# Kernel optimization log

Hardware: AMD Instinct MI355X
Metric: run time of the kernel (lower is better)

The kernel has to match this reference:

```python
import jax, jax.numpy as jnp
import numpy as np

NUM_NODES = 100000
NUM_EDGES = 1200000
DIM = 64
NUM_LAYERS = 3
NUM_GRAPHS = 512
BN_EPS = 1e-5


def setup_inputs() -> dict:
    key = jax.random.key(0)
    ks = jax.random.split(key, 12)
    x = jax.random.normal(ks[0], (NUM_NODES, DIM), dtype=jnp.float32)
    edge_index = jax.random.randint(ks[1], (2, NUM_EDGES), 0, NUM_NODES, dtype=jnp.int64)
    edge_weight = jax.random.uniform(ks[2], (NUM_EDGES,), dtype=jnp.float32)
    batch = jnp.sort(jax.random.randint(ks[3], (NUM_NODES,), 0, NUM_GRAPHS, dtype=jnp.int64))
    W1 = jax.random.normal(ks[4], (NUM_LAYERS, DIM, DIM), dtype=jnp.float32) * 0.1
    b1 = jax.random.normal(ks[5], (NUM_LAYERS, DIM), dtype=jnp.float32) * 0.1
    W2 = jax.random.normal(ks[6], (NUM_LAYERS, DIM, DIM), dtype=jnp.float32) * 0.1
    b2 = jax.random.normal(ks[7], (NUM_LAYERS, DIM), dtype=jnp.float32) * 0.1
    gamma = jax.random.uniform(ks[8], (NUM_LAYERS, DIM), dtype=jnp.float32) + 0.5
    beta = jax.random.normal(ks[9], (NUM_LAYERS, DIM), dtype=jnp.float32) * 0.1
    return {"x": x, "edge_index": edge_index, "edge_weight": edge_weight,
            "batch": batch, "pool": 0, "W1": W1, "b1": b1, "W2": W2,
            "b2": b2, "gamma": gamma, "beta": beta}


def reference(x, edge_index, edge_weight, batch, pool, W1, b1, W2, b2, gamma, beta):
    # WGINConv (eps=0): h = MLP(x + scatter_add(edge_weight * x[src] -> dst))
    # then ReLU, then BatchNorm1d in training mode (batch statistics).
    src, dst = edge_index[0], edge_index[1]
    n_nodes = x.shape[0]
    xs = []
    for i in range(W1.shape[0]):
        msg = x[src] * edge_weight[:, None]                       # [E, D] gather
        agg = jax.ops.segment_sum(msg, dst, num_segments=n_nodes)  # [N, D] scatter-add
        h = agg + x                                                # (1+eps)*x, eps=0
        h = jax.nn.relu(h @ W1[i].T + b1[i]) @ W2[i].T + b2[i]     # GIN MLP
        h = jax.nn.relu(h)
        mu = h.mean(0)
        var = ((h - mu) ** 2).mean(0)                              # biased var (BN train)
        x = gamma[i] * (h - mu) * jax.lax.rsqrt(var + BN_EPS) + beta[i]
        xs.append(x)
    if pool == 0:  # 'add' pooling (static python int)
        xpool = [jax.ops.segment_sum(v, batch, num_segments=NUM_GRAPHS) for v in xs]
    else:          # 'mean' pooling
        counts = jax.ops.segment_sum(jnp.ones((n_nodes,), x.dtype), batch,
                                     num_segments=NUM_GRAPHS)
        denom = jnp.maximum(counts, 1.0)[:, None]
        xpool = [jax.ops.segment_sum(v, batch, num_segments=NUM_GRAPHS) / denom for v in xs]
    return (jnp.concatenate(xpool, axis=1), jnp.concatenate(xs, axis=1))
```

## Files before the change

kernel.cpp:

```cpp
#include <hip/hip_runtime.h>

#define N_NODES 100000
#define N_EDGES 1200000
#define DIM     64
#define N_LAYERS 3
#define N_GRAPHS 512
#define OUTD    192
#define BN_EPS  1e-5f

#define NPB 64
#define LDS_PITCH 65
#define NLBLK ((N_NODES + NPB - 1) / NPB)

#define BSHIFT 9
#define BUCK_NODES (1 << BSHIFT)
#define NBUK ((N_NODES + BUCK_NODES - 1) / BUCK_NODES)
#define EPB 4096
#define NPBLK ((N_EDGES + EPB - 1) / EPB)

__global__ void transpose_w(const float* __restrict__ W1, const float* __restrict__ W2,
                            float* __restrict__ W1T, float* __restrict__ W2T,
                            float* __restrict__ idaff) {
    int idx = blockIdx.x * blockDim.x + threadIdx.x;
    if (idx < 128) idaff[idx] = (idx < 64) ? 1.0f : 0.0f;
    if (idx >= N_LAYERS * DIM * DIM) return;
    int l = idx >> 12;
    int r = idx & 4095;
    int j = r >> 6;
    int k = r & 63;
    int dstp = (l << 12) + k * DIM + j;
    W1T[dstp] = W1[idx];
    W2T[dstp] = W2[idx];
}

__global__ void __launch_bounds__(256) part_hist(const int* __restrict__ dst,
                                                 int* __restrict__ hist,
                                                 int* __restrict__ tot) {
    __shared__ int h[NBUK];
    int t = threadIdx.x;
    if (t < NBUK) h[t] = 0;
    __syncthreads();
    int base = blockIdx.x * EPB;
    for (int i = t; i < EPB; i += 256) {
        int e = base + i;
        if (e < N_EDGES) atomicAdd(&h[dst[e] >> BSHIFT], 1);
    }
    __syncthreads();
    if (t < NBUK) {
        int v = h[t];
        hist[blockIdx.x * NBUK + t] = v;
        if (v) atomicAdd(&tot[t], v);
    }
}

__global__ void __launch_bounds__(256) scan196(const int* __restrict__ tot,
                                               int* __restrict__ bstart) {
    __shared__ int lds[256];
    int t = threadIdx.x;
    int v = (t < NBUK) ? tot[t] : 0;
    lds[t] = v;
    __syncthreads();
    for (int o = 1; o < 256; o <<= 1) {
        int add = (t >= o) ? lds[t - o] : 0;
        __syncthreads();
        lds[t] += add;
        __syncthreads();
    }
    if (t < NBUK) bstart[t] = lds[t] - v;
    if (t == 0) bstart[NBUK] = N_EDGES;
}

__global__ void __launch_bounds__(256) base_fill(const int* __restrict__ hist,
                                                 const int* __restrict__ bstart,
                                                 int* __restrict__ base) {
    __shared__ int c[512];
    __shared__ int ssum[256];
    int b = blockIdx.x, t = threadIdx.x;
    c[t] = (t < NPBLK) ? hist[t * NBUK + b] : 0;
    c[t + 256] = (t + 256 < NPBLK) ? hist[(t + 256) * NBUK + b] : 0;
    __syncthreads();
    int c0 = c[2 * t], c1 = c[2 * t + 1];
    int ps = c0 + c1;
    ssum[t] = ps;
    __syncthreads();
    int v = ps;
    for (int o = 1; o < 256; o <<= 1) {
        int add = (t >= o) ? ssum[t - o] : 0;
        __syncthreads();
        ssum[t] += add;
        __syncthreads();
    }
    int excl = ssum[t] - v + bstart[b];
    if (2 * t < NPBLK)     base[(2 * t) * NBUK + b] = excl;
    if (2 * t + 1 < NPBLK) base[(2 * t + 1) * NBUK + b] = excl + c0;
}

__global__ void __launch_bounds__(256) part_scatter(
        const int* __restrict__ src, const int* __restrict__ dst,
        const float* __restrict__ ew, const int* __restrict__ base,
        int2* __restrict__ pp) {
    __shared__ int cur[NBUK];
    int t = threadIdx.x;
    if (t < NBUK) cur[t] = base[blockIdx.x * NBUK + t];
    __syncthreads();
    int bb = blockIdx.x * EPB;
    for (int i = t; i < EPB; i += 256) {
        int e = bb + i;
        if (e < N_EDGES) {
            int d = dst[e];
            int bk = d >> BSHIFT;
            int pos = atomicAdd(&cur[bk], 1);
            int dl = d & (BUCK_NODES - 1);
            pp[pos] = make_int2(src[e] | (dl << 17), __float_as_int(ew[e]));
        }
    }
}

__global__ void __launch_bounds__(256) csr_build(
        const int2* __restrict__ pp, const int* __restrict__ bstart,
        int* __restrict__ seg, int2* __restrict__ pe) {
    __shared__ int cnt[BUCK_NODES];
    __shared__ int ssum[256];
    int b = blockIdx.x, t = threadIdx.x;
    int ebeg = bstart[b], eend = bstart[b + 1];
    cnt[t] = 0;
    cnt[t + 256] = 0;
    __syncthreads();
    for (int e = ebeg + t; e < eend; e += 256)
        atomicAdd(&cnt[pp[e].x >> 17], 1);
    __syncthreads();
    int c0 = cnt[2 * t], c1 = cnt[2 * t + 1];
    int ps = c0 + c1;
    ssum[t] = ps;
    __syncthreads();
    int v = ps;
    for (int o = 1; o < 256; o <<= 1) {
        int add = (t >= o) ? ssum[t - o] : 0;
        __syncthreads();
        ssum[t] += add;
        __syncthreads();
    }
    int excl = ssum[t] - v;
    int o0 = ebeg + excl;
    int o1 = o0 + c0;
    int n0 = (b << BSHIFT) + 2 * t;
    if (n0 < N_NODES) seg[n0] = o0;
    if (n0 + 1 < N_NODES) seg[n0 + 1] = o1;
    __syncthreads();
    cnt[2 * t] = o0;
    cnt[2 * t + 1] = o1;
    __syncthreads();
    for (int e = ebeg + t; e < eend; e += 256) {
        int2 p = pp[e];
        int pos = atomicAdd(&cnt[p.x >> 17], 1);
        pe[pos] = make_int2(p.x & 0x1FFFF, p.y);
    }
    if (b == 0 && t == 0) seg[N_NODES] = N_EDGES;
}

__global__ void __launch_bounds__(256) layer_kernel(
    const float* __restrict__ x_in, int xstride,
    const int* __restrict__ seg,
    const int2* __restrict__ pe,
    const float* __restrict__ affine ,
    const float* __restrict__ W1T, const float* __restrict__ b1,
    const float* __restrict__ W2T, const float* __restrict__ b2,
    float* __restrict__ out ,
    float* __restrict__ pstat ) {
    __shared__ float lds[NPB * LDS_PITCH];
    int t = threadIdx.x;
    int lane = t & 63;
    int wid = __builtin_amdgcn_readfirstlane(t >> 6);
    int nbase = blockIdx.x * NPB;

    int slot = lane >> 4;
    int col  = lane & 15;
    const float4* aff4 = (const float4*)affine;
    float4 sc4 = aff4[col];
    float4 sh4 = aff4[16 + col];

    for (int nn = 0; nn < 16; ++nn) {
        int nl = wid * 16 + nn;
        int n = nbase + nl;
        float ax = 0.f, ay = 0.f, az = 0.f, aw = 0.f, wsa = 0.f;
        float bx = 0.f, by = 0.f, bz = 0.f, bw = 0.f, wsb = 0.f;
        if (n < N_NODES) {
            int beg = seg[n];
            int end = seg[n + 1];
#define GBODY(EI, X, Y, Z, W, WS)                                              \
            if ((EI) < end) {                                                  \
                int2 p = pe[EI];                                               \
                float w = __int_as_float(p.y);                                 \
                const float4* rp =                                             \
                    (const float4*)(x_in + (size_t)p.x * xstride) + col;       \
                float4 v = *rp;                                                \
                X = fmaf(w, v.x, X); Y = fmaf(w, v.y, Y);                      \
                Z = fmaf(w, v.z, Z); W = fmaf(w, v.w, W);                      \
                WS += w;                                                       \
            }
            for (int e = beg; e < end; e += 16) {
                int e0 = e + slot;
                GBODY(e0,      ax, ay, az, aw, wsa)
                GBODY(e0 + 4,  bx, by, bz, bw, wsb)
                GBODY(e0 + 8,  ax, ay, az, aw, wsa)
                GBODY(e0 + 12, bx, by, bz, bw, wsb)
            }
#undef GBODY
        }
        float sx = ax + bx, sy = ay + by, sz = az + bz, sw = aw + bw;
        float ws = wsa + wsb;
        sx += __shfl_xor(sx, 16); sy += __shfl_xor(sy, 16);
        sz += __shfl_xor(sz, 16); sw += __shfl_xor(sw, 16);
        ws += __shfl_xor(ws, 16);
        sx += __shfl_xor(sx, 32); sy += __shfl_xor(sy, 32);
        sz += __shfl_xor(sz, 32); sw += __shfl_xor(sw, 32);
        ws += __shfl_xor(ws, 32);
        if (lane < 16) {
            float r0 = 0.f, r1 = 0.f, r2 = 0.f, r3 = 0.f;
            if (n < N_NODES) {
                const float4* xr =
                    (const float4*)(x_in + (size_t)n * xstride) + col;
                float4 s = *xr;
                float shw = 1.0f + ws;
                r0 = fmaf(sc4.x, sx + s.x, sh4.x * shw);
                r1 = fmaf(sc4.y, sy + s.y, sh4.y * shw);
                r2 = fmaf(sc4.z, sz + s.z, sh4.z * shw);
                r3 = fmaf(sc4.w, sw + s.w, sh4.w * shw);
            }
            int lb = nl * LDS_PITCH + col * 4;
            lds[lb] = r0; lds[lb + 1] = r1; lds[lb + 2] = r2; lds[lb + 3] = r3;
        }
    }
    __syncthreads();

    float h[16];
#pragma unroll
    for (int jj = 0; jj < 16; ++jj) h[jj] = b1[wid * 16 + jj];
#pragma unroll 4
    for (int k = 0; k < DIM; ++k) {
        float xv = lds[lane * LDS_PITCH + k];
        const float* wr = W1T + k * DIM + wid * 16;
#pragma unroll
        for (int jj = 0; jj < 16; ++jj) h[jj] = fmaf(xv, wr[jj], h[jj]);
    }
#pragma unroll
    for (int jj = 0; jj < 16; ++jj) h[jj] = fmaxf(h[jj], 0.0f);
    __syncthreads();
#pragma unroll
    for (int jj = 0; jj < 16; ++jj) lds[lane * LDS_PITCH + wid * 16 + jj] = h[jj];
    __syncthreads();

    float o[16];
#pragma unroll
    for (int jj = 0; jj < 16; ++jj) o[jj] = b2[wid * 16 + jj];
#pragma unroll 4
    for (int k = 0; k < DIM; ++k) {
        float hv = lds[lane * LDS_PITCH + k];
        const float* wr = W2T + k * DIM + wid * 16;
#pragma unroll
        for (int jj = 0; jj < 16; ++jj) o[jj] = fmaf(hv, wr[jj], o[jj]);
    }
    int n = nbase + lane;
    bool valid = (n < N_NODES);
#pragma unroll
    for (int jj = 0; jj < 16; ++jj) o[jj] = fmaxf(o[jj], 0.0f);
    if (valid) {
        float* orow = out + (size_t)n * OUTD + wid * 16;
#pragma unroll
        for (int jj = 0; jj < 16; jj += 4) {
            *(float4*)(orow + jj) = make_float4(o[jj], o[jj + 1], o[jj + 2], o[jj + 3]);
        }
    }

    float my_s = 0.0f, my_q = 0.0f;
#pragma unroll
    for (int jj = 0; jj < 16; ++jj) {
        float v = valid ? o[jj] : 0.0f;
        float vs = v, vq = v * v;
#pragma unroll
        for (int m = 1; m < 64; m <<= 1) {
            vs += __shfl_xor(vs, m);
            vq += __shfl_xor(vq, m);
        }
        if (lane == jj) { my_s = vs; my_q = vq; }
    }
    if (lane < 16) {
        size_t base = (size_t)blockIdx.x * 128 + wid * 16 + lane;
        pstat[base] = my_s;
        pstat[base + 64] = my_q;
    }
}

__global__ void __launch_bounds__(256) reduce_stats(
    const float* __restrict__ pstat,
    const float* __restrict__ gamma, const float* __restrict__ beta,
    float* __restrict__ ss ) {
    __shared__ double part[16][16];
    int b = blockIdx.x;
    int t = threadIdx.x;
    int slot = t & 15;
    int g = t >> 4;
    int d = b * 8 + (slot & 7);
    int off = (slot < 8) ? 0 : 64;
    double s = 0.0;
    for (int blk = g; blk < NLBLK; blk += 16)
        s += (double)pstat[(size_t)blk * 128 + off + d];
    part[g][slot] = s;
    __syncthreads();
    if (t < 16) {
        double x = 0.0;
#pragma unroll
        for (int k = 0; k < 16; ++k) x += part[k][t];
        part[0][t] = x;
    }
    __syncthreads();
    if (t < 8) {
        int dd = b * 8 + t;
        double mu = part[0][t] / (double)N_NODES;
        double var = part[0][8 + t] / (double)N_NODES - mu * mu;
        float inv = (float)(1.0 / sqrt(var + (double)BN_EPS));
        float sc = gamma[dd] * inv;
        ss[dd] = sc;
        ss[64 + dd] = beta[dd] - (float)mu * sc;
    }
}

__global__ void bn_pool(float* __restrict__ xs,
                        const int* __restrict__ batch,
                        const float* __restrict__ ss ,
                        float* __restrict__ pooled) {
    int g = blockIdx.x;
    int part = blockIdx.y;
    int d = threadIdx.x;
    int l = d >> 6, dd = d & 63;
    float sc = ss[l * 128 + dd];
    float sh = ss[l * 128 + 64 + dd];
    int start, end;
    {
        int lo = 0, hi = N_NODES;
        while (lo < hi) { int m = (lo + hi) >> 1; if (batch[m] < g) lo = m + 1; else hi = m; }
        start = lo;
    }
    {
        int lo = start, hi = N_NODES;
        while (lo < hi) { int m = (lo + hi) >> 1; if (batch[m] <= g) lo = m + 1; else hi = m; }
        end = lo;
    }
    float acc = 0.0f;
    for (int n = start + part; n < end; n += 4) {
        float* p = xs + (size_t)n * OUTD + d;
        float v = fmaf(*p, sc, sh);
        *p = v;
        acc += v;
    }
    atomicAdd(&pooled[(size_t)g * OUTD + d], acc);
}

extern "C" void kernel_launch(void* const* d_in, const int* in_sizes, int n_in,
                              void* d_out, int out_size, void* d_ws, size_t ws_size,
                              hipStream_t stream) {
    const float* x0    = (const float*)d_in[0];
    const int*   ei    = (const int*)d_in[1];
    const float* ew    = (const float*)d_in[2];
    const int*   batch = (const int*)d_in[3];
    const float* W1    = (const float*)d_in[5];
    const float* b1    = (const float*)d_in[6];
    const float* W2    = (const float*)d_in[7];
    const float* b2    = (const float*)d_in[8];
    const float* gamma = (const float*)d_in[9];
    const float* beta  = (const float*)d_in[10];

    float* pooled = (float*)d_out;
    float* xs     = pooled + (size_t)N_GRAPHS * OUTD;

    const int* src = ei;
    const int* dst = ei + N_EDGES;

    int2*  pe     = (int2*)d_ws;
    int2*  pp     = pe + N_EDGES;
    int*   seg    = (int*)(pp + N_EDGES);
    int*   hist   = seg + N_NODES + 4;
    int*   pbase  = hist + (size_t)NPBLK * NBUK;
    int*   tot    = pbase + (size_t)NPBLK * NBUK;
    int*   bstart = tot + NBUK + 4;
    float* W1T    = (float*)(bstart + NBUK + 4);
    float* W2T    = W1T + N_LAYERS * DIM * DIM;
    float* idaff  = W2T + N_LAYERS * DIM * DIM;
    float* ss     = idaff + 128;
    float* pstat  = ss + N_LAYERS * 128;

    transpose_w<<<(N_LAYERS * DIM * DIM + 255) / 256, 256, 0, stream>>>(
        W1, W2, W1T, W2T, idaff);

    hipMemsetAsync(tot, 0, (NBUK + 4) * sizeof(int), stream);
    part_hist<<<NPBLK, 256, 0, stream>>>(dst, hist, tot);
    scan196<<<1, 256, 0, stream>>>(tot, bstart);
    base_fill<<<NBUK, 256, 0, stream>>>(hist, bstart, pbase);
    part_scatter<<<NPBLK, 256, 0, stream>>>(src, dst, ew, pbase, pp);
    csr_build<<<NBUK, 256, 0, stream>>>(pp, bstart, seg, pe);

    for (int i = 0; i < N_LAYERS; ++i) {
        const float* xin = (i == 0) ? x0 : (xs + (size_t)(i - 1) * DIM);
        int xstride = (i == 0) ? DIM : OUTD;
        const float* affine = (i == 0) ? idaff : (ss + (size_t)(i - 1) * 128);

        layer_kernel<<<NLBLK, 256, 0, stream>>>(
            xin, xstride, seg, pe, affine,
            W1T + (size_t)i * DIM * DIM, b1 + (size_t)i * DIM,
            W2T + (size_t)i * DIM * DIM, b2 + (size_t)i * DIM,
            xs + (size_t)i * DIM, pstat);

        reduce_stats<<<8, 256, 0, stream>>>(
            pstat, gamma + (size_t)i * DIM, beta + (size_t)i * DIM,
            ss + (size_t)i * 128);
    }

    hipMemsetAsync(pooled, 0, (size_t)N_GRAPHS * OUTD * sizeof(float), stream);
    dim3 pgrid(N_GRAPHS, 4);
    bn_pool<<<pgrid, OUTD, 0, stream>>>(xs, batch, ss, pooled);
}
```

Baseline: 537.9 us.

## Split fused layer kernel into separate gather and MLP kernels

Splits the per-layer kernel into a gather kernel and an MLP kernel. The gather kernel gives each node 16 lanes and walks its edges sequentially with 4-way unrolled independent loads, replacing the old scheme of one wave per 16 nodes processed one after another with shuffle reductions. The MLP kernel then reads the aggregated rows from a global buffer that reuses the CSR scratch area. The aim is more parallelism and memory-level concurrency in the gather, paid for by an extra global write and read of the aggregate and one more launch per layer.

```diff
diff --git a/kernel.cpp b/kernel.cpp
--- a/kernel.cpp
+++ b/kernel.cpp
@@ -11,6 +11,7 @@
 #define NPB 64
 #define LDS_PITCH 65
 #define NLBLK ((N_NODES + NPB - 1) / NPB)
+#define NGBLK ((N_NODES + 15) / 16)
 
 #define BSHIFT 9
 #define BUCK_NODES (1 << BSHIFT)
@@ -158,11 +159,67 @@
     if (b == 0 && t == 0) seg[N_NODES] = N_EDGES;
 }
 
-__global__ void __launch_bounds__(256) layer_kernel(
+__global__ void __launch_bounds__(256) gather_kernel(
     const float* __restrict__ x_in, int xstride,
-    const int* __restrict__ seg,
-    const int2* __restrict__ pe,
+    const int* __restrict__ seg, const int2* __restrict__ pe,
     const float* __restrict__ affine ,
+    float* __restrict__ agg ) {
+    int t = threadIdx.x;
+    int col = t & 15;
+    int n = blockIdx.x * 16 + (t >> 4);
+    if (n >= N_NODES) return;
+    const float4* aff4 = (const float4*)affine;
+    float4 sc4 = aff4[col];
+    float4 sh4 = aff4[16 + col];
+    int beg = seg[n], end = seg[n + 1];
+    float4 self = ((const float4*)(x_in + (size_t)n * xstride))[col];
+    float4 a0 = make_float4(0.f, 0.f, 0.f, 0.f);
+    float4 a1 = a0, a2 = a0, a3 = a0;
+    float w0s = 0.f, w1s = 0.f, w2s = 0.f, w3s = 0.f;
+    int e = beg;
+    for (; e + 4 <= end; e += 4) {
+        int2 p0 = pe[e];     int2 p1 = pe[e + 1];
+        int2 p2 = pe[e + 2]; int2 p3 = pe[e + 3];
+        float w0 = __int_as_float(p0.y), w1 = __int_as_float(p1.y);
+        float w2 = __int_as_float(p2.y), w3 = __int_as_float(p3.y);
+        float4 v0 = ((const float4*)(x_in + (size_t)p0.x * xstride))[col];
+        float4 v1 = ((const float4*)(x_in + (size_t)p1.x * xstride))[col];
+        float4 v2 = ((const float4*)(x_in + (size_t)p2.x * xstride))[col];
+        float4 v3 = ((const float4*)(x_in + (size_t)p3.x * xstride))[col];
+        a0.x = fmaf(w0, v0.x, a0.x); a0.y = fmaf(w0, v0.y, a0.y);
+        a0.z = fmaf(w0, v0.z, a0.z); a0.w = fmaf(w0, v0.w, a0.w);
+        a1.x = fmaf(w1, v1.x, a1.x); a1.y = fmaf(w1, v1.y, a1.y);
+        a1.z = fmaf(w1, v1.z, a1.z); a1.w = fmaf(w1, v1.w, a1.w);
+        a2.x = fmaf(w2, v2.x, a2.x); a2.y = fmaf(w2, v2.y, a2.y);
+        a2.z = fmaf(w2, v2.z, a2.z); a2.w = fmaf(w2, v2.w, a2.w);
+        a3.x = fmaf(w3, v3.x, a3.x); a3.y = fmaf(w3, v3.y, a3.y);
+        a3.z = fmaf(w3, v3.z, a3.z); a3.w = fmaf(w3, v3.w, a3.w);
+        w0s += w0; w1s += w1; w2s += w2; w3s += w3;
+    }
+    for (; e < end; ++e) {
+        int2 p = pe[e];
+        float w = __int_as_float(p.y);
+        float4 v = ((const float4*)(x_in + (size_t)p.x * xstride))[col];
+        a0.x = fmaf(w, v.x, a0.x); a0.y = fmaf(w, v.y, a0.y);
+        a0.z = fmaf(w, v.z, a0.z); a0.w = fmaf(w, v.w, a0.w);
+        w0s += w;
+    }
+    float4 s;
+    s.x = (a0.x + a1.x) + (a2.x + a3.x);
+    s.y = (a0.y + a1.y) + (a2.y + a3.y);
+    s.z = (a0.z + a1.z) + (a2.z + a3.z);
+    s.w = (a0.w + a1.w) + (a2.w + a3.w);
+    float shw = 1.0f + ((w0s + w1s) + (w2s + w3s));
+    float4 r;
+    r.x = fmaf(sc4.x, s.x + self.x, sh4.x * shw);
+    r.y = fmaf(sc4.y, s.y + self.y, sh4.y * shw);
+    r.z = fmaf(sc4.z, s.z + self.z, sh4.z * shw);
+    r.w = fmaf(sc4.w, s.w + self.w, sh4.w * shw);
+    ((float4*)(agg + (size_t)n * DIM))[col] = r;
+}
+
+__global__ void __launch_bounds__(256) mlp_kernel(
+    const float* __restrict__ agg,
     const float* __restrict__ W1T, const float* __restrict__ b1,
     const float* __restrict__ W2T, const float* __restrict__ b2,
     float* __restrict__ out ,
@@ -172,64 +229,18 @@
     int lane = t & 63;
     int wid = __builtin_amdgcn_readfirstlane(t >> 6);
     int nbase = blockIdx.x * NPB;
-
-    int slot = lane >> 4;
-    int col  = lane & 15;
-    const float4* aff4 = (const float4*)affine;
-    float4 sc4 = aff4[col];
-    float4 sh4 = aff4[16 + col];
-
-    for (int nn = 0; nn < 16; ++nn) {
-        int nl = wid * 16 + nn;
-        int n = nbase + nl;
-        float ax = 0.f, ay = 0.f, az = 0.f, aw = 0.f, wsa = 0.f;
-        float bx = 0.f, by = 0.f, bz = 0.f, bw = 0.f, wsb = 0.f;
-        if (n < N_NODES) {
-            int beg = seg[n];
-            int end = seg[n + 1];
-#define GBODY(EI, X, Y, Z, W, WS)                                              \
-            if ((EI) < end) {                                                  \
-                int2 p = pe[EI];                                               \
-                float w = __int_as_float(p.y);                                 \
-                const float4* rp =                                             \
-                    (const float4*)(x_in + (size_t)p.x * xstride) + col;       \
-                float4 v = *rp;                                                \
-                X = fmaf(w, v.x, X); Y = fmaf(w, v.y, Y);                      \
-                Z = fmaf(w, v.z, Z); W = fmaf(w, v.w, W);                      \
-                WS += w;                                                       \
-            }
-            for (int e = beg; e < end; e += 16) {
-                int e0 = e + slot;
-                GBODY(e0,      ax, ay, az, aw, wsa)
-                GBODY(e0 + 4,  bx, by, bz, bw, wsb)
-                GBODY(e0 + 8,  ax, ay, az, aw, wsa)
-                GBODY(e0 + 12, bx, by, bz, bw, wsb)
-            }
-#undef GBODY
-        }
-        float sx = ax + bx, sy = ay + by, sz = az + bz, sw = aw + bw;
-        float ws = wsa + wsb;
-        sx += __shfl_xor(sx, 16); sy += __shfl_xor(sy, 16);
-        sz += __shfl_xor(sz, 16); sw += __shfl_xor(sw, 16);
-        ws += __shfl_xor(ws, 16);
-        sx += __shfl_xor(sx, 32); sy += __shfl_xor(sy, 32);
-        sz += __shfl_xor(sz, 32); sw += __shfl_xor(sw, 32);
-        ws += __shfl_xor(ws, 32);
-        if (lane < 16) {
-            float r0 = 0.f, r1 = 0.f, r2 = 0.f, r3 = 0.f;
-            if (n < N_NODES) {
-                const float4* xr =
-                    (const float4*)(x_in + (size_t)n * xstride) + col;
-                float4 s = *xr;
-                float shw = 1.0f + ws;
-                r0 = fmaf(sc4.x, sx + s.x, sh4.x * shw);
-                r1 = fmaf(sc4.y, sy + s.y, sh4.y * shw);
-                r2 = fmaf(sc4.z, sz + s.z, sh4.z * shw);
-                r3 = fmaf(sc4.w, sw + s.w, sh4.w * shw);
-            }
-            int lb = nl * LDS_PITCH + col * 4;
-            lds[lb] = r0; lds[lb + 1] = r1; lds[lb + 2] = r2; lds[lb + 3] = r3;
-        }
+    int nvalid = N_NODES - nbase;
+    if (nvalid > NPB) nvalid = NPB;
+    int limit4 = nvalid * 16;
+
+    const float4* ag4 = (const float4*)(agg + (size_t)nbase * DIM);
+#pragma unroll
+    for (int k = 0; k < 4; ++k) {
+        int idx = t + k * 256;
+        float4 v = (idx < limit4) ? ag4[idx] : make_float4(0.f, 0.f, 0.f, 0.f);
+        int row = idx >> 4, c4 = idx & 15;
+        int lb = row * LDS_PITCH + c4 * 4;
+        lds[lb] = v.x; lds[lb + 1] = v.y; lds[lb + 2] = v.z; lds[lb + 3] = v.w;
     }
     __syncthreads();
 
@@ -377,17 +388,19 @@
     const int* dst = ei + N_EDGES;
 
     int2*  pe     = (int2*)d_ws;
-    int2*  pp     = pe + N_EDGES;
-    int*   seg    = (int*)(pp + N_EDGES);
-    int*   hist   = seg + N_NODES + 4;
-    int*   pbase  = hist + (size_t)NPBLK * NBUK;
-    int*   tot    = pbase + (size_t)NPBLK * NBUK;
+    int*   seg    = (int*)(pe + N_EDGES);
+    int*   tot    = seg + N_NODES + 4;
     int*   bstart = tot + NBUK + 4;
     float* W1T    = (float*)(bstart + NBUK + 4);
     float* W2T    = W1T + N_LAYERS * DIM * DIM;
     float* idaff  = W2T + N_LAYERS * DIM * DIM;
     float* ss     = idaff + 128;
     float* pstat  = ss + N_LAYERS * 128;
+    float* uni    = pstat + (size_t)NLBLK * 128;
+    int2*  pp     = (int2*)uni;
+    int*   hist   = (int*)(pp + N_EDGES);
+    int*   pbase  = hist + (size_t)NPBLK * NBUK;
+    float* agg    = uni;
 
     transpose_w<<<(N_LAYERS * DIM * DIM + 255) / 256, 256, 0, stream>>>(
         W1, W2, W1T, W2T, idaff);
@@ -404,8 +417,11 @@
         int xstride = (i == 0) ? DIM : OUTD;
         const float* affine = (i == 0) ? idaff : (ss + (size_t)(i - 1) * 128);
 
-        layer_kernel<<<NLBLK, 256, 0, stream>>>(
-            xin, xstride, seg, pe, affine,
+        gather_kernel<<<NGBLK, 256, 0, stream>>>(
+            xin, xstride, seg, pe, affine, agg);
+
+        mlp_kernel<<<NLBLK, 256, 0, stream>>>(
+            agg,
             W1T + (size_t)i * DIM * DIM, b1 + (size_t)i * DIM,
             W2T + (size_t)i * DIM * DIM, b2 + (size_t)i * DIM,
             xs + (size_t)i * DIM, pstat);
```

After: 557.6 us. +3.7%, slower.

## Gather neighbor features from a bf16 shadow copy to halve gather bandwidth

Applied to the files above, without the earlier changes.

Adds a bf16 copy of each layer's input features: one conversion kernel for x0, and for layers 0 and 1 the layer kernel also writes a bf16 version of its output. The edge-gather loop then reads 8-byte ushort4 rows instead of 16-byte float4 rows, cutting the dominant random-gather memory traffic roughly in half. The bf16 buffers reuse the workspace region of the partition scratch arrays once the CSR is built. In exchange, neighbor features are rounded to bf16, which may push results past tolerance, and there are extra write passes.

```diff
diff --git a/kernel.cpp b/kernel.cpp
--- a/kernel.cpp
+++ b/kernel.cpp
@@ -17,6 +17,14 @@
 #define NBUK ((N_NODES + BUCK_NODES - 1) / BUCK_NODES)
 #define EPB 4096
 #define NPBLK ((N_EDGES + EPB - 1) / EPB)
+
+__device__ __forceinline__ unsigned short f2bf(float f) {
+    unsigned u = __float_as_uint(f);
+    return (unsigned short)((u + 0x7FFFu + ((u >> 16) & 1u)) >> 16);
+}
+__device__ __forceinline__ float bf2f(unsigned short h) {
+    return __uint_as_float(((unsigned)h) << 16);
+}
 
 __global__ void transpose_w(const float* __restrict__ W1, const float* __restrict__ W2,
                             float* __restrict__ W1T, float* __restrict__ W2T,
@@ -33,6 +41,16 @@
     W2T[dstp] = W2[idx];
 }
 
+__global__ void __launch_bounds__(256) to_bf16(const float* __restrict__ x,
+                                               unsigned short* __restrict__ x16) {
+    int i = blockIdx.x * blockDim.x + threadIdx.x;
+    if (i >= N_NODES * 16) return;
+    float4 v = ((const float4*)x)[i];
+    ushort4 r;
+    r.x = f2bf(v.x); r.y = f2bf(v.y); r.z = f2bf(v.z); r.w = f2bf(v.w);
+    ((ushort4*)x16)[i] = r;
+}
+
 __global__ void __launch_bounds__(256) part_hist(const int* __restrict__ dst,
                                                  int* __restrict__ hist,
                                                  int* __restrict__ tot) {
@@ -160,6 +178,8 @@
 
 __global__ void __launch_bounds__(256) layer_kernel(
     const float* __restrict__ x_in, int xstride,
+    const unsigned short* __restrict__ x16in,
+    unsigned short* __restrict__ x16out, int wr16,
     const int* __restrict__ seg,
     const int2* __restrict__ pe,
     const float* __restrict__ affine ,
@@ -191,11 +211,10 @@
             if ((EI) < end) {                                                  \
                 int2 p = pe[EI];                                               \
                 float w = __int_as_float(p.y);                                 \
-                const float4* rp =                                             \
-                    (const float4*)(x_in + (size_t)p.x * xstride) + col;       \
-                float4 v = *rp;                                                \
-                X = fmaf(w, v.x, X); Y = fmaf(w, v.y, Y);                      \
-                Z = fmaf(w, v.z, Z); W = fmaf(w, v.w, W);                      \
+                ushort4 hv =                                                   \
+                    ((const ushort4*)(x16in + (size_t)p.x * DIM))[col];        \
+                X = fmaf(w, bf2f(hv.x), X); Y = fmaf(w, bf2f(hv.y), Y);        \
+                Z = fmaf(w, bf2f(hv.z), Z); W = fmaf(w, bf2f(hv.w), W);        \
                 WS += w;                                                       \
             }
             for (int e = beg; e < end; e += 16) {
@@ -270,6 +289,16 @@
         for (int jj = 0; jj < 16; jj += 4) {
             *(float4*)(orow + jj) = make_float4(o[jj], o[jj + 1], o[jj + 2], o[jj + 3]);
         }
+        if (wr16) {
+            unsigned short* hrow = x16out + (size_t)n * DIM + wid * 16;
+#pragma unroll
+            for (int jj = 0; jj < 16; jj += 4) {
+                ushort4 hq;
+                hq.x = f2bf(o[jj]);     hq.y = f2bf(o[jj + 1]);
+                hq.z = f2bf(o[jj + 2]); hq.w = f2bf(o[jj + 3]);
+                *(ushort4*)(hrow + jj) = hq;
+            }
+        }
     }
 
     float my_s = 0.0f, my_q = 0.0f;
@@ -377,17 +406,20 @@
     const int* dst = ei + N_EDGES;
 
     int2*  pe     = (int2*)d_ws;
-    int2*  pp     = pe + N_EDGES;
-    int*   seg    = (int*)(pp + N_EDGES);
-    int*   hist   = seg + N_NODES + 4;
-    int*   pbase  = hist + (size_t)NPBLK * NBUK;
-    int*   tot    = pbase + (size_t)NPBLK * NBUK;
+    int*   seg    = (int*)(pe + N_EDGES);
+    int*   tot    = seg + N_NODES + 4;
     int*   bstart = tot + NBUK + 4;
     float* W1T    = (float*)(bstart + NBUK + 4);
     float* W2T    = W1T + N_LAYERS * DIM * DIM;
     float* idaff  = W2T + N_LAYERS * DIM * DIM;
     float* ss     = idaff + 128;
     float* pstat  = ss + N_LAYERS * 128;
+    char* uni = (char*)(pstat + (size_t)NLBLK * 128);
+    int2*  pp     = (int2*)uni;
+    int*   hist   = (int*)(pp + N_EDGES);
+    int*   pbase  = hist + (size_t)NPBLK * NBUK;
+    unsigned short* x16a = (unsigned short*)uni;
+    unsigned short* x16b = x16a + (size_t)N_NODES * DIM;
 
     transpose_w<<<(N_LAYERS * DIM * DIM + 255) / 256, 256, 0, stream>>>(
         W1, W2, W1T, W2T, idaff);
@@ -399,13 +431,18 @@
     part_scatter<<<NPBLK, 256, 0, stream>>>(src, dst, ew, pbase, pp);
     csr_build<<<NBUK, 256, 0, stream>>>(pp, bstart, seg, pe);
 
+    to_bf16<<<(N_NODES * 16 + 255) / 256, 256, 0, stream>>>(x0, x16a);
+
     for (int i = 0; i < N_LAYERS; ++i) {
         const float* xin = (i == 0) ? x0 : (xs + (size_t)(i - 1) * DIM);
         int xstride = (i == 0) ? DIM : OUTD;
         const float* affine = (i == 0) ? idaff : (ss + (size_t)(i - 1) * 128);
+        const unsigned short* x16in = (i == 1) ? x16b : x16a;
+        unsigned short* x16out = (i == 0) ? x16b : x16a;
+        int wr16 = (i < N_LAYERS - 1) ? 1 : 0;
 
         layer_kernel<<<NLBLK, 256, 0, stream>>>(
-            xin, xstride, seg, pe, affine,
+            xin, xstride, x16in, x16out, wr16, seg, pe, affine,
             W1T + (size_t)i * DIM * DIM, b1 + (size_t)i * DIM,
             W2T + (size_t)i * DIM * DIM, b2 + (size_t)i * DIM,
             xs + (size_t)i * DIM, pstat);
```

Result: no change. 539.4 us (+0.3%).
